# Optimization experiments

Hardware: AMD Instinct MI355X
Metric: run time of the kernel (lower is better)

Reference implementation:

```python
import jax, jax.numpy as jnp
import numpy as np

N = 20000      # nodes
E = 320000     # edges (before self-loops)
IN = 128       # input_dim
HID = 64       # hidden_dim
HEADS = 4      # num_heads
SLOPE = 0.2    # PyG GATConv leaky_relu negative_slope


def setup_inputs() -> dict:
    key = jax.random.key(0)
    ks = jax.random.split(key, 20)
    g = lambda k, shape: jax.random.normal(k, shape, dtype=jnp.float32) * 0.1
    return {
        "x": jax.random.normal(ks[0], (N, IN), dtype=jnp.float32),
        "edge_index": jax.random.randint(ks[1], (2, E), 0, N),
        # layer 0: IN -> HID x HEADS, concat
        "lin0": g(ks[2], (IN, HEADS * HID)),
        "att_src0": g(ks[3], (HEADS, HID)),
        "att_dst0": g(ks[4], (HEADS, HID)),
        "bias0": g(ks[5], (HEADS * HID,)),
        # layer 1: HID*HEADS -> HID x HEADS, concat
        "lin1": g(ks[6], (HEADS * HID, HEADS * HID)),
        "att_src1": g(ks[7], (HEADS, HID)),
        "att_dst1": g(ks[8], (HEADS, HID)),
        "bias1": g(ks[9], (HEADS * HID,)),
        # layer 2: HID*HEADS -> HID, 1 head, mean (concat=False)
        "lin2": g(ks[10], (HEADS * HID, HID)),
        "att_src2": g(ks[11], (1, HID)),
        "att_dst2": g(ks[12], (1, HID)),
        "bias2": g(ks[13], (HID,)),
        # output MLP: HID -> HID//2 -> 1
        "w1": g(ks[14], (HID, HID // 2)),
        "b1": g(ks[15], (HID // 2,)),
        "w2": g(ks[16], (HID // 2, 1)),
        "b2": g(ks[17], (1,)),
    }


def _gat(x, src, dst, lin, att_src, att_dst, bias, heads, concat):
    n = x.shape[0]
    ch = att_src.shape[1]
    h = (x @ lin).reshape(n, heads, ch)                       # [N,H,C]
    a_s = jnp.sum(h * att_src, axis=-1)                       # [N,H]
    a_d = jnp.sum(h * att_dst, axis=-1)                       # [N,H]
    e = jax.nn.leaky_relu(a_s[src] + a_d[dst], negative_slope=SLOPE)  # [E,H]
    emax = jax.ops.segment_max(e, dst, num_segments=n)        # segment softmax over dst
    ee = jnp.exp(e - emax[dst])
    denom = jax.ops.segment_sum(ee, dst, num_segments=n)
    alpha = ee / denom[dst]                                   # [E,H]
    out = jax.ops.segment_sum(h[src] * alpha[:, :, None], dst, num_segments=n)  # [N,H,C]
    out = out.reshape(n, heads * ch) if concat else jnp.mean(out, axis=1)
    return out + bias


def reference(x, edge_index, lin0, att_src0, att_dst0, bias0,
              lin1, att_src1, att_dst1, bias1,
              lin2, att_src2, att_dst2, bias2,
              w1, b1, w2, b2):
    n = x.shape[0]
    loops = jnp.arange(n, dtype=edge_index.dtype)
    edge = jnp.concatenate([edge_index, jnp.stack([loops, loops])], axis=1)  # add self loops
    src, dst = edge[0], edge[1]
    h = jax.nn.elu(_gat(x, src, dst, lin0, att_src0, att_dst0, bias0, HEADS, True))
    h = jax.nn.elu(_gat(h, src, dst, lin1, att_src1, att_dst1, bias1, HEADS, True))
    h = jax.nn.elu(_gat(h, src, dst, lin2, att_src2, att_dst2, bias2, 1, False))
    h = jax.nn.relu(h @ w1 + b1)
    return h @ w2 + b2
```

## Files before the change

### kernel.cpp

```cpp
#include <hip/hip_runtime.h>

#define NNODES 20000
#define NEDGES 320000
#define ELLW 64
#define DCAP 64

typedef __attribute__((ext_vector_type(4))) float f32x4;
typedef _Float16 f16x4 __attribute__((ext_vector_type(4)));
typedef _Float16 f16x8 __attribute__((ext_vector_type(8)));

__device__ __forceinline__ float leaky(float x) { return x > 0.f ? x : 0.2f * x; }
__device__ __forceinline__ float elu(float x) { return x > 0.f ? x : expm1f(x); }

__device__ __forceinline__ void gll16(const ushort* g, ushort* l) {
  __builtin_amdgcn_global_load_lds((const __attribute__((address_space(1))) void*)g,
                                   (__attribute__((address_space(3))) void*)l, 16, 0, 0);
}

__device__ __forceinline__ void prep_w_one(const float* __restrict__ w, _Float16* __restrict__ th,
                                           int K, int OC, int idx) {
  int KC = K / 32;
  int oc = idx / KC, c = idx % KC;
  _Float16 h[32];
#pragma unroll
  for (int r = 0; r < 32; r++) {
    int p = (r < 16) ? ((r >> 2) * 8 + (r & 3)) : (((r - 16) >> 2) * 8 + 4 + (r & 3));
    h[p] = (_Float16)w[(size_t)(c * 32 + r) * OC + oc];
  }
  _Float16* ho = th + (size_t)oc * K + c * 32;
#pragma unroll
  for (int q = 0; q < 4; q++) *(f16x8*)&ho[q * 8] = *(f16x8*)&h[q * 8];
}

__global__ void k_prep_w3z(const float* __restrict__ w0, const float* __restrict__ w1,
                           const float* __restrict__ w2,
                           _Float16* __restrict__ th0, _Float16* __restrict__ th1,
                           _Float16* __restrict__ th2, int* __restrict__ fill) {
  int i = blockIdx.x * blockDim.x + threadIdx.x;
  if (i < NNODES) fill[i] = 0;
  if (i < 1024) prep_w_one(w0, th0, 128, 256, i);
  else if (i < 3072) prep_w_one(w1, th1, 256, 256, i - 1024);
  else if (i < 3584) prep_w_one(w2, th2, 256, 64, i - 3072);
}

__global__ void k_cvt_ell(const float* __restrict__ a, _Float16* __restrict__ Ap, int total,
                          const int* __restrict__ srcA, const int* __restrict__ dstA,
                          int* __restrict__ fill, int* __restrict__ ell, int e) {
  int i = blockIdx.x * blockDim.x + threadIdx.x;
  if (i < e) {
    int d = dstA[i];
    int k = atomicAdd(&fill[d], 1);
    if (k < ELLW) ell[d * ELLW + k] = srcA[i];
  }
  if (i >= total) return;
  const float* src = a + (size_t)i * 32;
  _Float16 h[32];
#pragma unroll
  for (int r = 0; r < 32; r++) {
    int p = (r < 16) ? ((r >> 2) * 8 + (r & 3)) : (((r - 16) >> 2) * 8 + 4 + (r & 3));
    h[p] = (_Float16)src[r];
  }
  _Float16* ho = Ap + (size_t)i * 32;
#pragma unroll
  for (int q = 0; q < 4; q++) *(f16x8*)&ho[q * 8] = *(f16x8*)&h[q * 8];
}

template <int K, int NCT, int HEADS>
__global__ __launch_bounds__(256) void k_gemm_mfma(const ushort* __restrict__ Ah, const ushort* __restrict__ Bh,
                                                   const float* __restrict__ asrc, const float* __restrict__ adst,
                                                   _Float16* __restrict__ H, float* __restrict__ a_s,
                                                   float* __restrict__ a_d, int M, int OC) {
  constexpr int BM = 64, BN = NCT * 64, NC = K / 32;
  constexpr int BOFF = 2048;
  constexpr int BUFE = BOFF + BN * 32;
  __shared__ ushort sb0[BUFE], sb1[BUFE];
  __shared__ float sh_s[4][64], sh_d[4][64];
  int w = threadIdx.x >> 6, l = threadIdx.x & 63;
  int n0 = blockIdx.x * BM;
  int cw = blockIdx.y * BN + w * (NCT * 16);
  int lr = l & 15;

  int q = l & 3;
  int srow = 16 * w + (l >> 2);
  int sgrow = min(n0 + srow, M - 1);
  int gA = q ^ ((srow >> 1) & 3);
  const ushort* aH = Ah + (size_t)sgrow * K + gA * 8;
  const ushort* bH[NCT];
  int colb[NCT];
#pragma unroll
  for (int i = 0; i < NCT; i++) {
    colb[i] = 16 * NCT * w + 16 * i;
    int sc = colb[i] + (l >> 2);
    int gB = q ^ ((sc >> 1) & 3);
    bH[i] = Bh + (size_t)(blockIdx.y * BN + sc) * K + gB * 8;
  }

#define STAGE(buf, c)                                              \
  {                                                                \
    gll16(aH + (c) * 32, &buf[w * 512]);                           \
    _Pragma("unroll") for (int i = 0; i < NCT; i++)                \
      gll16(bH[i] + (c) * 32, &buf[BOFF + colb[i] * 32]);          \
  }

  f32x4 acc[4][NCT];
#pragma unroll
  for (int r = 0; r < 4; r++)
#pragma unroll
    for (int t = 0; t < NCT; t++) acc[r][t] = (f32x4){0.f, 0.f, 0.f, 0.f};

#define COMP(buf)                                                                   \
  {                                                                                 \
    f16x8 bhf[NCT];                                                                 \
    _Pragma("unroll") for (int t = 0; t < NCT; t++) {                               \
      int bcol = 16 * NCT * w + 16 * t + lr;                                        \
      int gb = (l >> 4) ^ ((bcol >> 1) & 3);                                        \
      bhf[t] = *(const f16x8*)&buf[BOFF + bcol * 32 + gb * 8];                      \
    }                                                                               \
    _Pragma("unroll") for (int r = 0; r < 4; r++) {                                 \
      int arow = 16 * r + lr;                                                       \
      int ga = (l >> 4) ^ ((arow >> 1) & 3);                                        \
      f16x8 ahf = *(const f16x8*)&buf[arow * 32 + ga * 8];                          \
      _Pragma("unroll") for (int t = 0; t < NCT; t++)                               \
        acc[r][t] = __builtin_amdgcn_mfma_f32_16x16x32_f16(ahf, bhf[t], acc[r][t], 0, 0, 0); \
    }                                                                               \
  }

  ushort* cur = sb0;
  ushort* nxt = sb1;
  STAGE(cur, 0);
  __syncthreads();
  for (int c = 0; c < NC; ++c) {
    if (c + 1 < NC) STAGE(nxt, c + 1);
    COMP(cur);
    __syncthreads();
    ushort* tmp = cur; cur = nxt; nxt = tmp;
  }
#undef STAGE
#undef COMP

#pragma unroll
  for (int r = 0; r < 4; r++)
#pragma unroll
    for (int t = 0; t < NCT; t++)
#pragma unroll
      for (int reg = 0; reg < 4; reg++) {
        int row = n0 + 16 * r + (l >> 4) * 4 + reg;
        if (row < M) H[(size_t)row * OC + cw + 16 * t + lr] = (_Float16)acc[r][t][reg];
      }

  float asv[NCT], adv[NCT];
#pragma unroll
  for (int t = 0; t < NCT; t++) {
    asv[t] = asrc[cw + 16 * t + lr];
    adv[t] = adst[cw + 16 * t + lr];
  }
#pragma unroll
  for (int r = 0; r < 4; r++) {
#pragma unroll
    for (int reg = 0; reg < 4; reg++) {
      float ps = 0.f, pd = 0.f;
#pragma unroll
      for (int t = 0; t < NCT; t++) {
        ps += acc[r][t][reg] * asv[t];
        pd += acc[r][t][reg] * adv[t];
      }
#pragma unroll
      for (int mask = 1; mask < 16; mask <<= 1) {
        ps += __shfl_xor(ps, mask, 64);
        pd += __shfl_xor(pd, mask, 64);
      }
      int rl = 16 * r + (l >> 4) * 4 + reg;
      if (lr == 0) { sh_s[w][rl] = ps; sh_d[w][rl] = pd; }
    }
  }
  __syncthreads();
  int tid = threadIdx.x;
  if (HEADS == 4) {
    if (tid < 128) {
      int rr = tid & 63, hl = tid >> 6;
      int row = n0 + rr;
      if (row < M) {
        int hidx = row * 4 + blockIdx.y * 2 + hl;
        a_s[hidx] = sh_s[2 * hl][rr] + sh_s[2 * hl + 1][rr];
        a_d[hidx] = sh_d[2 * hl][rr] + sh_d[2 * hl + 1][rr];
      }
    }
  } else {
    if (tid < 64) {
      int row = n0 + tid;
      if (row < M) {
        a_s[row] = sh_s[0][tid] + sh_s[1][tid] + sh_s[2][tid] + sh_s[3][tid];
        a_d[row] = sh_d[0][tid] + sh_d[1][tid] + sh_d[2][tid] + sh_d[3][tid];
      }
    }
  }
}

__global__ __launch_bounds__(256) void k_gat4(const _Float16* __restrict__ h, const float* __restrict__ a_s,
                                              const float* __restrict__ a_d, const int* __restrict__ fill,
                                              const int* __restrict__ ell, const float* __restrict__ bias,
                                              _Float16* __restrict__ Ap) {
  __shared__ float elds[4][DCAP * 4];
  int wid = threadIdx.x >> 6, l = threadIdx.x & 63;
  int n = blockIdx.x * 4 + wid;
  if (n >= NNODES) return;
  int head = l >> 4, sub = l & 15;
  int half = l >> 5, sl = l & 31;
  int head2 = sl >> 3;
  int jb = n * ELLW;
  int cnt = min(fill[n], ELLW);
  int je = jb + cnt;
  float ad = a_d[n * 4 + head];
  float es = leaky(a_s[n * 4 + head] + ad);
  float m = -1e30f, s = 0.f;
  if (sub == 0) { m = es; s = 1.f; }
  for (int j = jb + sub; j < je; j += 16) {
    float e = leaky(a_s[ell[j] * 4 + head] + ad);
    elds[wid][(j - jb) * 4 + head] = e;
    float nm = fmaxf(m, e);
    s = s * __expf(m - nm) + __expf(e - nm);
    m = nm;
  }
#pragma unroll
  for (int mask = 1; mask < 16; mask <<= 1) {
    float m2 = __shfl_xor(m, mask, 64);
    float s2 = __shfl_xor(s, mask, 64);
    float nm = fmaxf(m, m2);
    s = s * __expf(m - nm) + s2 * __expf(m2 - nm);
    m = nm;
  }
  __asm__ volatile("" ::: "memory");
  float inv = 1.f / s;
  float sa = __expf(es - m) * inv;
  int srcl = head2 << 4;
  float m2r = __shfl(m, srcl, 64);
  float inv2 = __shfl(inv, srcl, 64);
  float sa2 = __shfl(sa, srcl, 64);

  float acc[8];
  f16x8 hv = *(const f16x8*)&h[(size_t)n * 256 + sl * 8];
#pragma unroll
  for (int i = 0; i < 8; i++) acc[i] = (half == 0) ? sa2 * (float)hv[i] : 0.f;

  int j = jb;
  for (; j + 7 < je; j += 8) {
    int e0 = j + half, e1 = j + 2 + half, e2 = j + 4 + half, e3 = j + 6 + half;
    int s0 = ell[e0], s1 = ell[e1], s2 = ell[e2], s3 = ell[e3];
    float a0 = __expf(elds[wid][(e0 - jb) * 4 + head2] - m2r) * inv2;
    float a1 = __expf(elds[wid][(e1 - jb) * 4 + head2] - m2r) * inv2;
    float a2 = __expf(elds[wid][(e2 - jb) * 4 + head2] - m2r) * inv2;
    float a3 = __expf(elds[wid][(e3 - jb) * 4 + head2] - m2r) * inv2;
    f16x8 v0 = *(const f16x8*)&h[(size_t)s0 * 256 + sl * 8];
    f16x8 v1 = *(const f16x8*)&h[(size_t)s1 * 256 + sl * 8];
    f16x8 v2 = *(const f16x8*)&h[(size_t)s2 * 256 + sl * 8];
    f16x8 v3 = *(const f16x8*)&h[(size_t)s3 * 256 + sl * 8];
#pragma unroll
    for (int i = 0; i < 8; i++)
      acc[i] += a0 * (float)v0[i] + a1 * (float)v1[i] + a2 * (float)v2[i] + a3 * (float)v3[i];
  }
  for (; j + 1 < je; j += 2) {
    int e0 = j + half;
    int s0 = ell[e0];
    float a0 = __expf(elds[wid][(e0 - jb) * 4 + head2] - m2r) * inv2;
    f16x8 v0 = *(const f16x8*)&h[(size_t)s0 * 256 + sl * 8];
#pragma unroll
    for (int i = 0; i < 8; i++) acc[i] += a0 * (float)v0[i];
  }
  if (j < je) {
    int s0 = ell[j];
    float a0 = (half == 0) ? __expf(elds[wid][(j - jb) * 4 + head2] - m2r) * inv2 : 0.f;
    f16x8 v0 = *(const f16x8*)&h[(size_t)s0 * 256 + sl * 8];
#pragma unroll
    for (int i = 0; i < 8; i++) acc[i] += a0 * (float)v0[i];
  }
#pragma unroll
  for (int i = 0; i < 8; i++) acc[i] += __shfl_xor(acc[i], 32, 64);

  int c0 = sl * 8 + half * 4;
  int k = c0 & 31;
  size_t base = (size_t)n * 256 + (c0 >> 5) * 32 + ((k < 16) ? (k >> 2) * 8 : (((k - 16) >> 2) * 8 + 4));
  float4 b = *(const float4*)&bias[c0];
  int ai = half * 4;
  f16x4 pk;
  pk[0] = (_Float16)elu(acc[ai + 0] + b.x);
  pk[1] = (_Float16)elu(acc[ai + 1] + b.y);
  pk[2] = (_Float16)elu(acc[ai + 2] + b.z);
  pk[3] = (_Float16)elu(acc[ai + 3] + b.w);
  *(f16x4*)&Ap[base] = pk;
}

__global__ __launch_bounds__(256) void k_gat1(const _Float16* __restrict__ h, const float* __restrict__ a_s,
                                              const float* __restrict__ a_d, const int* __restrict__ fill,
                                              const int* __restrict__ ell, const float* __restrict__ bias,
                                              const float* __restrict__ w1, const float* __restrict__ b1,
                                              const float* __restrict__ w2, const float* __restrict__ b2,
                                              float* __restrict__ out) {
  __shared__ float elds[4][DCAP];
  __shared__ float sh[4][64];
  int wid = threadIdx.x >> 6, l = threadIdx.x & 63;
  int n = blockIdx.x * 4 + wid;
  int grp = l >> 4, cl = l & 15;
  float acc[4] = {0.f, 0.f, 0.f, 0.f};
  if (n < NNODES) {
    int jb = n * ELLW;
    int cnt = min(fill[n], ELLW);
    int je = jb + cnt;
    float ad = a_d[n];
    float es = leaky(a_s[n] + ad);
    float m = -1e30f, s = 0.f;
    if (l == 0) { m = es; s = 1.f; }
    for (int j = jb + l; j < je; j += 64) {
      float e = leaky(a_s[ell[j]] + ad);
      elds[wid][j - jb] = e;
      float nm = fmaxf(m, e);
      s = s * __expf(m - nm) + __expf(e - nm);
      m = nm;
    }
#pragma unroll
    for (int mask = 1; mask < 64; mask <<= 1) {
      float m2 = __shfl_xor(m, mask, 64);
      float s2 = __shfl_xor(s, mask, 64);
      float nm = fmaxf(m, m2);
      s = s * __expf(m - nm) + s2 * __expf(m2 - nm);
      m = nm;
    }
    __asm__ volatile("" ::: "memory");
    float inv = 1.f / s;
    float sa = __expf(es - m) * inv;
    f16x4 hv = *(const f16x4*)&h[(size_t)n * 64 + cl * 4];
    if (grp == 0) {
#pragma unroll
      for (int i = 0; i < 4; i++) acc[i] = sa * (float)hv[i];
    }
    int j = jb;
    for (; j + 7 < je; j += 8) {
      int e0 = j + grp, e1 = j + 4 + grp;
      int s0 = ell[e0], s1 = ell[e1];
      float a0 = __expf(elds[wid][e0 - jb] - m) * inv;
      float a1 = __expf(elds[wid][e1 - jb] - m) * inv;
      f16x4 v0 = *(const f16x4*)&h[(size_t)s0 * 64 + cl * 4];
      f16x4 v1 = *(const f16x4*)&h[(size_t)s1 * 64 + cl * 4];
#pragma unroll
      for (int i = 0; i < 4; i++) acc[i] += a0 * (float)v0[i] + a1 * (float)v1[i];
    }
    for (; j + 3 < je; j += 4) {
      int e0 = j + grp;
      int s0 = ell[e0];
      float a0 = __expf(elds[wid][e0 - jb] - m) * inv;
      f16x4 v0 = *(const f16x4*)&h[(size_t)s0 * 64 + cl * 4];
#pragma unroll
      for (int i = 0; i < 4; i++) acc[i] += a0 * (float)v0[i];
    }
    if (j + grp < je) {
      int e0 = j + grp;
      int s0 = ell[e0];
      float a0 = __expf(elds[wid][e0 - jb] - m) * inv;
      f16x4 v0 = *(const f16x4*)&h[(size_t)s0 * 64 + cl * 4];
#pragma unroll
      for (int i = 0; i < 4; i++) acc[i] += a0 * (float)v0[i];
    }
  }
#pragma unroll
  for (int i = 0; i < 4; i++) {
    acc[i] += __shfl_xor(acc[i], 16, 64);
    acc[i] += __shfl_xor(acc[i], 32, 64);
  }
  if (n < NNODES && l < 16) {
#pragma unroll
    for (int i = 0; i < 4; i++) sh[wid][cl * 4 + i] = elu(acc[i] + bias[cl * 4 + i]);
  }
  __syncthreads();
  float r = 0.f;
  if (l < 32 && n < NNODES) {
    r = b1[l];
#pragma unroll 8
    for (int k = 0; k < 64; k++) r += sh[wid][k] * w1[k * 32 + l];
    r = fmaxf(r, 0.f);
    r *= w2[l];
  }
  for (int mask = 16; mask >= 1; mask >>= 1) r += __shfl_xor(r, mask, 64);
  if (l == 0 && n < NNODES) out[n] = r + b2[0];
}

extern "C" void kernel_launch(void* const* d_in, const int* in_sizes, int n_in,
                              void* d_out, int out_size, void* d_ws, size_t ws_size,
                              hipStream_t stream) {
  const float* x    = (const float*)d_in[0];
  const int*   eidx = (const int*)d_in[1];
  const float* lin0 = (const float*)d_in[2];
  const float* as0  = (const float*)d_in[3];
  const float* ad0  = (const float*)d_in[4];
  const float* b0   = (const float*)d_in[5];
  const float* lin1 = (const float*)d_in[6];
  const float* as1  = (const float*)d_in[7];
  const float* ad1  = (const float*)d_in[8];
  const float* b1l  = (const float*)d_in[9];
  const float* lin2 = (const float*)d_in[10];
  const float* as2  = (const float*)d_in[11];
  const float* ad2  = (const float*)d_in[12];
  const float* b2l  = (const float*)d_in[13];
  const float* w1   = (const float*)d_in[14];
  const float* mb1  = (const float*)d_in[15];
  const float* w2   = (const float*)d_in[16];
  const float* mb2  = (const float*)d_in[17];
  float* outp = (float*)d_out;

  const int* srcA = eidx;
  const int* dstA = eidx + NEDGES;

  char* ws = (char*)d_ws;
  size_t o = 0;
  auto alloc = [&](size_t bytes) { size_t r = o; o += (bytes + 255) & ~255UL; return r; };
  _Float16* h16 = (_Float16*)(ws + alloc((size_t)NNODES * 256 * 2));
  _Float16* Ap  = (_Float16*)(ws + alloc((size_t)NNODES * 256 * 2));
  _Float16* wh0 = (_Float16*)(ws + alloc(128 * 256 * 2));
  _Float16* wh1 = (_Float16*)(ws + alloc(256 * 256 * 2));
  _Float16* wh2 = (_Float16*)(ws + alloc(256 * 64 * 2));
  float*  vas = (float*)(ws + alloc((size_t)NNODES * 4 * 4));
  float*  vad = (float*)(ws + alloc((size_t)NNODES * 4 * 4));
  int* fill = (int*)(ws + alloc(NNODES * 4));
  int* ell  = (int*)(ws + alloc((size_t)NNODES * ELLW * 4));

  k_prep_w3z<<<(NNODES + 255) / 256, 256, 0, stream>>>(lin0, lin1, lin2, wh0, wh1, wh2, fill);
  k_cvt_ell<<<(NEDGES + 255) / 256, 256, 0, stream>>>(x, Ap, NNODES * 4, srcA, dstA, fill, ell, NEDGES);

  dim3 g44((NNODES + 63) / 64, 2);
  dim3 g21((NNODES + 63) / 64, 1);

  k_gemm_mfma<128, 2, 4><<<g44, 256, 0, stream>>>((const ushort*)Ap, (const ushort*)wh0, as0, ad0, h16, vas, vad, NNODES, 256);
  k_gat4<<<5000, 256, 0, stream>>>(h16, vas, vad, fill, ell, b0, Ap);

  k_gemm_mfma<256, 2, 4><<<g44, 256, 0, stream>>>((const ushort*)Ap, (const ushort*)wh1, as1, ad1, h16, vas, vad, NNODES, 256);
  k_gat4<<<5000, 256, 0, stream>>>(h16, vas, vad, fill, ell, b1l, Ap);

  k_gemm_mfma<256, 1, 1><<<g21, 256, 0, stream>>>((const ushort*)Ap, (const ushort*)wh2, as2, ad2, h16, vas, vad, NNODES, 64);
  k_gat1<<<5000, 256, 0, stream>>>(h16, vas, vad, fill, ell, b2l, w1, mb1, w2, mb2, outp);
}
```

Measured before the change: 152.4 us.

## Split 4-head GAT aggregation into one wavefront per node per head

```diff
diff --git a/kernel.cpp b/kernel.cpp
--- a/kernel.cpp
+++ b/kernel.cpp
@@ -196,33 +196,32 @@
   }
 }
 
-__global__ __launch_bounds__(256) void k_gat4(const _Float16* __restrict__ h, const float* __restrict__ a_s,
-                                              const float* __restrict__ a_d, const int* __restrict__ fill,
-                                              const int* __restrict__ ell, const float* __restrict__ bias,
-                                              _Float16* __restrict__ Ap) {
-  __shared__ float elds[4][DCAP * 4];
+__global__ __launch_bounds__(256) void k_gat4h(const _Float16* __restrict__ h, const float* __restrict__ a_s,
+                                               const float* __restrict__ a_d, const int* __restrict__ fill,
+                                               const int* __restrict__ ell, const float* __restrict__ bias,
+                                               _Float16* __restrict__ Ap) {
+  __shared__ float elds[4][DCAP];
   int wid = threadIdx.x >> 6, l = threadIdx.x & 63;
   int n = blockIdx.x * 4 + wid;
   if (n >= NNODES) return;
-  int head = l >> 4, sub = l & 15;
-  int half = l >> 5, sl = l & 31;
-  int head2 = sl >> 3;
+  int hd = blockIdx.y;
+  int grp = l >> 4, cl = l & 15;
   int jb = n * ELLW;
   int cnt = min(fill[n], ELLW);
   int je = jb + cnt;
-  float ad = a_d[n * 4 + head];
-  float es = leaky(a_s[n * 4 + head] + ad);
+  float ad = a_d[n * 4 + hd];
+  float es = leaky(a_s[n * 4 + hd] + ad);
   float m = -1e30f, s = 0.f;
-  if (sub == 0) { m = es; s = 1.f; }
-  for (int j = jb + sub; j < je; j += 16) {
-    float e = leaky(a_s[ell[j] * 4 + head] + ad);
-    elds[wid][(j - jb) * 4 + head] = e;
+  if (l == 0) { m = es; s = 1.f; }
+  for (int j = jb + l; j < je; j += 64) {
+    float e = leaky(a_s[ell[j] * 4 + hd] + ad);
+    elds[wid][j - jb] = e;
     float nm = fmaxf(m, e);
     s = s * __expf(m - nm) + __expf(e - nm);
     m = nm;
   }
 #pragma unroll
-  for (int mask = 1; mask < 16; mask <<= 1) {
+  for (int mask = 1; mask < 64; mask <<= 1) {
     float m2 = __shfl_xor(m, mask, 64);
     float s2 = __shfl_xor(s, mask, 64);
     float nm = fmaxf(m, m2);
@@ -232,61 +231,58 @@
   __asm__ volatile("" ::: "memory");
   float inv = 1.f / s;
   float sa = __expf(es - m) * inv;
-  int srcl = head2 << 4;
-  float m2r = __shfl(m, srcl, 64);
-  float inv2 = __shfl(inv, srcl, 64);
-  float sa2 = __shfl(sa, srcl, 64);
-
-  float acc[8];
-  f16x8 hv = *(const f16x8*)&h[(size_t)n * 256 + sl * 8];
-#pragma unroll
-  for (int i = 0; i < 8; i++) acc[i] = (half == 0) ? sa2 * (float)hv[i] : 0.f;
-
+
+  const _Float16* hh = h + hd * 64;
+  float acc[4] = {0.f, 0.f, 0.f, 0.f};
+  f16x4 hv = *(const f16x4*)&hh[(size_t)n * 256 + cl * 4];
+  if (grp == 0) {
+#pragma unroll
+    for (int i = 0; i < 4; i++) acc[i] = sa * (float)hv[i];
+  }
   int j = jb;
   for (; j + 7 < je; j += 8) {
-    int e0 = j + half, e1 = j + 2 + half, e2 = j + 4 + half, e3 = j + 6 + half;
-    int s0 = ell[e0], s1 = ell[e1], s2 = ell[e2], s3 = ell[e3];
-    float a0 = __expf(elds[wid][(e0 - jb) * 4 + head2] - m2r) * inv2;
-    float a1 = __expf(elds[wid][(e1 - jb) * 4 + head2] - m2r) * inv2;
-    float a2 = __expf(elds[wid][(e2 - jb) * 4 + head2] - m2r) * inv2;
-    float a3 = __expf(elds[wid][(e3 - jb) * 4 + head2] - m2r) * inv2;
-    f16x8 v0 = *(const f16x8*)&h[(size_t)s0 * 256 + sl * 8];
-    f16x8 v1 = *(const f16x8*)&h[(size_t)s1 * 256 + sl * 8];
-    f16x8 v2 = *(const f16x8*)&h[(size_t)s2 * 256 + sl * 8];
-    f16x8 v3 = *(const f16x8*)&h[(size_t)s3 * 256 + sl * 8];
-#pragma unroll
-    for (int i = 0; i < 8; i++)
-      acc[i] += a0 * (float)v0[i] + a1 * (float)v1[i] + a2 * (float)v2[i] + a3 * (float)v3[i];
-  }
-  for (; j + 1 < je; j += 2) {
-    int e0 = j + half;
+    int e0 = j + grp, e1 = j + 4 + grp;
+    int s0 = ell[e0], s1 = ell[e1];
+    float a0 = __expf(elds[wid][e0 - jb] - m) * inv;
+    float a1 = __expf(elds[wid][e1 - jb] - m) * inv;
+    f16x4 v0 = *(const f16x4*)&hh[(size_t)s0 * 256 + cl * 4];
+    f16x4 v1 = *(const f16x4*)&hh[(size_t)s1 * 256 + cl * 4];
+#pragma unroll
+    for (int i = 0; i < 4; i++) acc[i] += a0 * (float)v0[i] + a1 * (float)v1[i];
+  }
+  for (; j + 3 < je; j += 4) {
+    int e0 = j + grp;
     int s0 = ell[e0];
-    float a0 = __expf(elds[wid][(e0 - jb) * 4 + head2] - m2r) * inv2;
-    f16x8 v0 = *(const f16x8*)&h[(size_t)s0 * 256 + sl * 8];
-#pragma unroll
-    for (int i = 0; i < 8; i++) acc[i] += a0 * (float)v0[i];
-  }
-  if (j < je) {
-    int s0 = ell[j];
-    float a0 = (half == 0) ? __expf(elds[wid][(j - jb) * 4 + head2] - m2r) * inv2 : 0.f;
-    f16x8 v0 = *(const f16x8*)&h[(size_t)s0 * 256 + sl * 8];
-#pragma unroll
-    for (int i = 0; i < 8; i++) acc[i] += a0 * (float)v0[i];
-  }
-#pragma unroll
-  for (int i = 0; i < 8; i++) acc[i] += __shfl_xor(acc[i], 32, 64);
-
-  int c0 = sl * 8 + half * 4;
-  int k = c0 & 31;
-  size_t base = (size_t)n * 256 + (c0 >> 5) * 32 + ((k < 16) ? (k >> 2) * 8 : (((k - 16) >> 2) * 8 + 4));
-  float4 b = *(const float4*)&bias[c0];
-  int ai = half * 4;
-  f16x4 pk;
-  pk[0] = (_Float16)elu(acc[ai + 0] + b.x);
-  pk[1] = (_Float16)elu(acc[ai + 1] + b.y);
-  pk[2] = (_Float16)elu(acc[ai + 2] + b.z);
-  pk[3] = (_Float16)elu(acc[ai + 3] + b.w);
-  *(f16x4*)&Ap[base] = pk;
+    float a0 = __expf(elds[wid][e0 - jb] - m) * inv;
+    f16x4 v0 = *(const f16x4*)&hh[(size_t)s0 * 256 + cl * 4];
+#pragma unroll
+    for (int i = 0; i < 4; i++) acc[i] += a0 * (float)v0[i];
+  }
+  if (j + grp < je) {
+    int e0 = j + grp;
+    int s0 = ell[e0];
+    float a0 = __expf(elds[wid][e0 - jb] - m) * inv;
+    f16x4 v0 = *(const f16x4*)&hh[(size_t)s0 * 256 + cl * 4];
+#pragma unroll
+    for (int i = 0; i < 4; i++) acc[i] += a0 * (float)v0[i];
+  }
+#pragma unroll
+  for (int i = 0; i < 4; i++) {
+    acc[i] += __shfl_xor(acc[i], 16, 64);
+    acc[i] += __shfl_xor(acc[i], 32, 64);
+  }
+  if (l < 16) {
+    int c0 = hd * 64 + cl * 4;
+    int k = c0 & 31;
+    size_t base = (size_t)n * 256 + (c0 >> 5) * 32 + ((k < 16) ? (k >> 2) * 8 : (((k - 16) >> 2) * 8 + 4));
+    float4 b = *(const float4*)&bias[c0];
+    f16x4 pk;
+    pk[0] = (_Float16)elu(acc[0] + b.x);
+    pk[1] = (_Float16)elu(acc[1] + b.y);
+    pk[2] = (_Float16)elu(acc[2] + b.z);
+    pk[3] = (_Float16)elu(acc[3] + b.w);
+    *(f16x4*)&Ap[base] = pk;
+  }
 }
 
 __global__ __launch_bounds__(256) void k_gat1(const _Float16* __restrict__ h, const float* __restrict__ a_s,
@@ -426,13 +422,14 @@
 
   dim3 g44((NNODES + 63) / 64, 2);
   dim3 g21((NNODES + 63) / 64, 1);
+  dim3 gg4((NNODES + 3) / 4, 4);
 
   k_gemm_mfma<128, 2, 4><<<g44, 256, 0, stream>>>((const ushort*)Ap, (const ushort*)wh0, as0, ad0, h16, vas, vad, NNODES, 256);
-  k_gat4<<<5000, 256, 0, stream>>>(h16, vas, vad, fill, ell, b0, Ap);
+  k_gat4h<<<gg4, 256, 0, stream>>>(h16, vas, vad, fill, ell, b0, Ap);
 
   k_gemm_mfma<256, 2, 4><<<g44, 256, 0, stream>>>((const ushort*)Ap, (const ushort*)wh1, as1, ad1, h16, vas, vad, NNODES, 256);
-  k_gat4<<<5000, 256, 0, stream>>>(h16, vas, vad, fill, ell, b1l, Ap);
+  k_gat4h<<<gg4, 256, 0, stream>>>(h16, vas, vad, fill, ell, b1l, Ap);
 
   k_gemm_mfma<256, 1, 1><<<g21, 256, 0, stream>>>((const ushort*)Ap, (const ushort*)wh2, as2, ad2, h16, vas, vad, NNODES, 64);
-  k_gat1<<<5000, 256, 0, stream>>>(h16, vas, vad, fill, ell, b2l, w1, mb1, w2, mb2, outp);
-}
+  k_gat1<<<(NNODES + 3) / 4, 256, 0, stream>>>(h16, vas, vad, fill, ell, b2l, w1, mb1, w2, mb2, outp);
+}
```

Result: slower. 203.9 us (+33.8%).
